# Optimization experiments

Measured on AMD Instinct MI355X. Metric: run time of the kernel, lower is better.

## Reference

```python
import jax, jax.numpy as jnp
import numpy as np

N_EMBD = 1024
N_FF = 4 * N_EMBD
N_EXPERTS = 8
TOP_K = 2
B, S = 1, 2048


def setup_inputs() -> dict:
    key = jax.random.key(0)
    ks = jax.random.split(key, 8)
    std = 0.02
    x = jax.random.normal(ks[0], (B, S, N_EMBD), dtype=jnp.float32)
    Wr = jax.random.normal(ks[1], (N_EMBD, N_EXPERTS), dtype=jnp.float32) * std
    br = jnp.zeros((N_EXPERTS,), dtype=jnp.float32)
    W1 = jax.random.normal(ks[2], (N_EXPERTS, N_EMBD, N_FF), dtype=jnp.float32) * std
    b1 = jnp.zeros((N_EXPERTS, N_FF), dtype=jnp.float32)
    W2 = jax.random.normal(ks[3], (N_EXPERTS, N_FF, N_EMBD), dtype=jnp.float32) * std
    b2 = jnp.zeros((N_EXPERTS, N_EMBD), dtype=jnp.float32)
    return {"x": x, "Wr": Wr, "br": br, "W1": W1, "b1": b1, "W2": W2, "b2": b2}


def reference(x, Wr, br, W1, b1, W2, b2):
    # x: [B, S, D]
    Bx, Sx, D = x.shape
    T = Bx * Sx
    E = Wr.shape[1]
    flat = x.reshape(T, D)

    # Router: softmax over experts, top-k, renormalize top-k weights
    logits = flat @ Wr + br                      # [T, E]
    probs = jax.nn.softmax(logits, axis=-1)
    topk_w, topk_i = jax.lax.top_k(probs, TOP_K)  # [T, K]
    topk_w = topk_w / jnp.sum(topk_w, axis=-1, keepdims=True)

    # Per-token combined expert weights (0 for non-selected experts).
    # Equivalent to the original gather/index_add combine.
    tok = jnp.arange(T)[:, None]
    w = jnp.zeros((T, E), dtype=flat.dtype).at[tok, topk_i].add(topk_w)  # [T, E]

    # Dense grouped expert MLP (exact GELU, matching torch nn.GELU default).
    h = jnp.einsum('td,edh->teh', flat, W1) + b1          # [T, E, 4D]
    h = jax.nn.gelu(h, approximate=False)
    y = jnp.einsum('teh,ehd->ted', h, W2) + b2            # [T, E, D]

    out = jnp.einsum('ted,te->td', y, w)                  # weighted combine
    return out.reshape(Bx, Sx, D)
```

## Files before the change

kernel.cpp:

```cpp
#include <hip/hip_runtime.h>
#include <stdint.h>

#define T_TOK 2048
#define DIM   1024
#define HID   4096
#define NEXP  8

typedef __attribute__((ext_vector_type(8))) short  short8;
typedef __attribute__((ext_vector_type(4))) short  short4v;
typedef __attribute__((ext_vector_type(4))) float  floatx4;
typedef __attribute__((ext_vector_type(4))) int    intx4;

__device__ __forceinline__ ushort f2bf(float f) {
    union { float f; uint32_t i; } v; v.f = f;
    uint32_t r = v.i + 0x7FFFu + ((v.i >> 16) & 1u);
    return (ushort)(r >> 16);
}
__device__ __forceinline__ float gelu_exact(float x) {
    return 0.5f * x * (1.0f + erff(x * 0.70710678118654752f));
}
__device__ __forceinline__ void glds16(const ushort* g, ushort* lds) {
    __builtin_amdgcn_global_load_lds(
        (const __attribute__((address_space(1))) unsigned int*)g,
        (__attribute__((address_space(3))) unsigned int*)lds, 16, 0, 0);
}

__global__ __launch_bounds__(256) void cast_x_kernel(
    const float* __restrict__ x, ushort* __restrict__ Xb)
{
    int i = (blockIdx.x * 256 + threadIdx.x) * 8;
    floatx4 a = *(const floatx4*)(x + i);
    floatx4 b = *(const floatx4*)(x + i + 4);
    uint32_t o[4];
    o[0] = (uint32_t)f2bf(a[0]) | ((uint32_t)f2bf(a[1]) << 16);
    o[1] = (uint32_t)f2bf(a[2]) | ((uint32_t)f2bf(a[3]) << 16);
    o[2] = (uint32_t)f2bf(b[0]) | ((uint32_t)f2bf(b[1]) << 16);
    o[3] = (uint32_t)f2bf(b[2]) | ((uint32_t)f2bf(b[3]) << 16);
    *(intx4*)(Xb + i) = *(const intx4*)o;
}

__global__ __launch_bounds__(256) void transpose_cast_kernel(
    const float* __restrict__ in, ushort* __restrict__ out, int R, int C)
{
    __shared__ float tile[64][65];
    int e = blockIdx.z;
    int rb = blockIdx.y * 64, cb = blockIdx.x * 64;
    const float* ip = in + (size_t)e * R * C;
    ushort* op = out + (size_t)e * R * C;
    int t = threadIdx.x;
    int tr = t >> 4, tc4 = (t & 15) * 4;
#pragma unroll
    for (int i = 0; i < 4; i++) {
        int r = i * 16 + tr;
        floatx4 v = *(const floatx4*)(ip + (size_t)(rb + r) * C + cb + tc4);
        tile[r][tc4] = v[0]; tile[r][tc4 + 1] = v[1];
        tile[r][tc4 + 2] = v[2]; tile[r][tc4 + 3] = v[3];
    }
    __syncthreads();
    int cc = t >> 2, rseg = (t & 3) * 16;
#pragma unroll
    for (int s = 0; s < 2; s++) {
        ushort o[8];
#pragma unroll
        for (int j = 0; j < 8; j++) o[j] = f2bf(tile[rseg + s * 8 + j][cc]);
        *(intx4*)(op + (size_t)(cb + cc) * R + rb + rseg + s * 8) = *(const intx4*)o;
    }
}

__global__ __launch_bounds__(256) void router_kernel(
    const float* __restrict__ x, const float* __restrict__ Wr,
    const float* __restrict__ br, int* __restrict__ counts,
    int* __restrict__ tlist, float* __restrict__ wlist)
{
    int wv = threadIdx.x >> 6, l = threadIdx.x & 63;
    int t = blockIdx.x * 4 + wv;
    float acc[NEXP];
#pragma unroll
    for (int e = 0; e < NEXP; e++) acc[e] = 0.f;
    const float* xr = x + (size_t)t * DIM;
    for (int d = l; d < DIM; d += 64) {
        float xv = xr[d];
        floatx4 w0 = *(const floatx4*)(Wr + (size_t)d * NEXP);
        floatx4 w1 = *(const floatx4*)(Wr + (size_t)d * NEXP + 4);
#pragma unroll
        for (int e = 0; e < 4; e++) { acc[e] += xv * w0[e]; acc[e + 4] += xv * w1[e]; }
    }
#pragma unroll
    for (int e = 0; e < NEXP; e++) {
#pragma unroll
        for (int off = 32; off; off >>= 1) acc[e] += __shfl_xor(acc[e], off, 64);
    }
    if (l == 0) {
        float lg[NEXP];
#pragma unroll
        for (int e = 0; e < NEXP; e++) lg[e] = acc[e] + br[e];
        int e0 = 0;
#pragma unroll
        for (int e = 1; e < NEXP; e++) if (lg[e] > lg[e0]) e0 = e;
        int e1 = -1;
#pragma unroll
        for (int e = 0; e < NEXP; e++) {
            if (e == e0) continue;
            if (e1 < 0 || lg[e] > lg[e1]) e1 = e;
        }
        float w0 = 1.f / (1.f + expf(lg[e1] - lg[e0]));
        float w1 = 1.f - w0;
        int s0 = atomicAdd(&counts[e0], 1);
        tlist[e0 * T_TOK + s0] = t;
        wlist[e0 * T_TOK + s0] = w0;
        int s1 = atomicAdd(&counts[e1], 1);
        tlist[e1 * T_TOK + s1] = t | (1 << 16);
        wlist[e1 * T_TOK + s1] = w1;
    }
}

template <int MODE>
__global__ __launch_bounds__(256, 2) void moe_gemm3(
    const ushort* __restrict__ A, const ushort* __restrict__ Wt,
    const float* __restrict__ bias, const int* __restrict__ counts,
    const int* __restrict__ tlist, const float* __restrict__ wlist,
    ushort* __restrict__ Hout, float* __restrict__ Yout)
{
    constexpr int NTOT  = MODE ? DIM : HID;
    constexpr int KFULL = MODE ? HID : DIM;
    constexpr int KLEN  = MODE ? 2048 : 1024;
    constexpr int NTILE = KLEN / 64;

    int bx = blockIdx.x;
    int e, mt, nt, kc;
    if (MODE == 0) { e = bx >> 9; mt = (bx >> 5) & 15; nt = bx & 31; kc = 0; }
    else { e = bx >> 8; int rr = bx & 255; mt = rr >> 4; nt = (rr >> 1) & 7; kc = rr & 1; }

    int Ne = counts[e];
    if (mt * 128 >= Ne) return;

    __shared__ ushort lds[32768];

    int tid = threadIdx.x, wv = tid >> 6, l = tid & 63;

    int s0 = mt * 128 + l;      if (s0 >= Ne) s0 = Ne - 1;
    int s1 = mt * 128 + 64 + l; if (s1 >= Ne) s1 = Ne - 1;
    int p0 = tlist[e * T_TOK + s0], p1 = tlist[e * T_TOK + s1];
    size_t ar0 = MODE ? (size_t)((p0 & 0xFFFF) * 2 + ((p0 >> 16) & 1)) : (size_t)(p0 & 0xFFFF);
    size_t ar1 = MODE ? (size_t)((p1 & 0xFFFF) * 2 + ((p1 >> 16) & 1)) : (size_t)(p1 & 0xFFFF);
    const ushort* asrc0 = A + ar0 * KFULL + kc * 2048;
    const ushort* asrc1 = A + ar1 * KFULL + kc * 2048;
    const ushort* bsrc0 = Wt + (size_t)e * NTOT * KFULL
                             + (size_t)(nt * 128 + l) * KFULL + kc * 2048;
    const ushort* bsrc1 = bsrc0 + (size_t)64 * KFULL;
    int q0 = wv, q1 = wv + 4;

#define STAGE(buf, t) do {                                             \
        ushort* Lb = &lds[(buf) * 16384];                              \
        int ko = (t) * 64;                                             \
        glds16(asrc0 + ko + q0 * 8, Lb + q0 * 1024);                   \
        glds16(asrc0 + ko + q1 * 8, Lb + q1 * 1024);                   \
        glds16(asrc1 + ko + q0 * 8, Lb + q0 * 1024 + 512);             \
        glds16(asrc1 + ko + q1 * 8, Lb + q1 * 1024 + 512);             \
        glds16(bsrc0 + ko + q0 * 8, Lb + 8192 + q0 * 1024);            \
        glds16(bsrc0 + ko + q1 * 8, Lb + 8192 + q1 * 1024);            \
        glds16(bsrc1 + ko + q0 * 8, Lb + 8192 + q0 * 1024 + 512);      \
        glds16(bsrc1 + ko + q1 * 8, Lb + 8192 + q1 * 1024 + 512);      \
    } while (0)

    int wm = wv >> 1, wn = wv & 1, q4 = l >> 4, lr = l & 15;
    int aro[4], bro[4];
#pragma unroll
    for (int mi = 0; mi < 4; mi++) aro[mi] = (wm * 64 + mi * 16 + lr) * 8;
#pragma unroll
    for (int ni = 0; ni < 4; ni++) bro[ni] = 8192 + (wn * 64 + ni * 16 + lr) * 8;

    floatx4 zz = {0.f, 0.f, 0.f, 0.f};
    floatx4 acc[4][4];
#pragma unroll
    for (int mi = 0; mi < 4; mi++)
#pragma unroll
        for (int ni = 0; ni < 4; ni++) acc[mi][ni] = zz;

    STAGE(0, 0);
    int cur = 0;
    for (int t = 0; t < NTILE; ++t) {
        asm volatile("" ::: "memory");
        __builtin_amdgcn_s_barrier();
        asm volatile("" ::: "memory");
        if (t + 1 < NTILE) {
            STAGE(cur ^ 1, t + 1);
            asm volatile("s_waitcnt vmcnt(8)" ::: "memory");
        } else {
            asm volatile("s_waitcnt vmcnt(0)" ::: "memory");
        }
        __builtin_amdgcn_s_barrier();
        asm volatile("" ::: "memory");

        const ushort* Lp = &lds[cur * 16384];
        short8 af[4], bfv[4];
#pragma unroll
        for (int kk = 0; kk < 2; ++kk) {
            int qb = (kk * 4 + q4) * 1024;
#pragma unroll
            for (int ni = 0; ni < 4; ni++) bfv[ni] = *(const short8*)&Lp[qb + bro[ni]];
#pragma unroll
            for (int mi = 0; mi < 4; mi++) af[mi] = *(const short8*)&Lp[qb + aro[mi]];
#pragma unroll
            for (int mi = 0; mi < 4; mi++)
#pragma unroll
                for (int ni = 0; ni < 4; ni++)
                    acc[mi][ni] = __builtin_amdgcn_mfma_f32_16x16x32_bf16(
                        af[mi], bfv[ni], acc[mi][ni], 0, 0, 0);
        }
        cur ^= 1;
    }
#undef STAGE

#pragma unroll
    for (int mi = 0; mi < 4; mi++) {
        int rbase = wm * 64 + mi * 16 + q4 * 4;
#pragma unroll
        for (int j = 0; j < 4; j++) {
            int slot2 = mt * 128 + rbase + j;
            if (slot2 >= Ne) continue;
            int pk2 = tlist[e * T_TOK + slot2];
            int tok2 = pk2 & 0xFFFF, rk2 = (pk2 >> 16) & 1;
#pragma unroll
            for (int ni = 0; ni < 4; ni++) {
                int col = nt * 128 + wn * 64 + ni * 16 + lr;
                float v = acc[mi][ni][j];
                float bc = bias[e * NTOT + col];
                if (MODE == 0) {
                    v = gelu_exact(v + bc);
                    Hout[(size_t)(tok2 * 2 + rk2) * HID + col] = f2bf(v);
                } else {
                    if (kc == 0) v += bc;
                    v *= wlist[e * T_TOK + slot2];
                    atomicAdd(&Yout[(size_t)tok2 * DIM + col], v);
                }
            }
        }
    }
}

template <int MODE>
__global__ __launch_bounds__(256, 2) void moe_gemm(
    const ushort* __restrict__ A, const float* __restrict__ W,
    const float* __restrict__ bias, const int* __restrict__ counts,
    const int* __restrict__ tlist, const float* __restrict__ wlist,
    ushort* __restrict__ Hout, float* __restrict__ Yacc)
{
    constexpr int NTOT = MODE ? DIM : HID;
    constexpr int AROW = MODE ? HID : DIM;
    constexpr int KLEN = MODE ? 2048 : 1024;

    int bx = blockIdx.x;
    int e, mt, nt, kc;
    if (MODE == 0) { e = bx >> 9; mt = (bx >> 5) & 15; nt = bx & 31; kc = 0; }
    else { e = bx >> 8; int r = bx & 255; mt = r >> 4; nt = (r >> 1) & 7; kc = r & 1; }

    int Ne = counts[e];
    if (mt * 128 >= Ne) return;

    size_t wbase = (size_t)e * DIM * HID + (size_t)kc * 2048 * NTOT + (size_t)nt * 128;

    __shared__ ushort ldsA[128 * 40];
    __shared__ ushort ldsB[128 * 36];

    int tid = threadIdx.x;
    int wv = tid >> 6, l = tid & 63;

    const ushort* arowp[2]; int apos[2];
#pragma unroll
    for (int i = 0; i < 2; i++) {
        int idx = i * 256 + tid;
        int r = idx >> 2, p = idx & 3;
        int slot = mt * 128 + r; if (slot >= Ne) slot = Ne - 1;
        int packed = tlist[e * T_TOK + slot];
        int tok = packed & 0xFFFF, rk = (packed >> 16) & 1;
        size_t arow = MODE ? (size_t)(tok * 2 + rk) : (size_t)tok;
        arowp[i] = A + arow * AROW + (MODE ? kc * 2048 : 0) + p * 8;
        apos[i] = r * 40 + p * 8;
    }

    int kp = tid & 15;
    int n8 = tid >> 4;
    size_t boffg = wbase + (size_t)(2 * kp) * NTOT + n8 * 8;

    int wm = wv >> 1, wn = wv & 1;
    int q = l >> 4;
    int aoff[4], boff[4];
#pragma unroll
    for (int mi = 0; mi < 4; mi++)
        aoff[mi] = (wm * 64 + mi * 16 + (l & 15)) * 40 + q * 8;
#pragma unroll
    for (int ni = 0; ni < 4; ni++)
        boff[ni] = (wn * 64 + ni * 16 + (l & 15)) * 36 + q * 8;

    floatx4 zz = {0.f, 0.f, 0.f, 0.f};
    floatx4 acc[4][4];
#pragma unroll
    for (int mi = 0; mi < 4; mi++)
#pragma unroll
        for (int ni = 0; ni < 4; ni++) acc[mi][ni] = zz;

    for (int k0 = 0; k0 < KLEN; k0 += 32) {
        intx4 av[2];
#pragma unroll
        for (int i = 0; i < 2; i++) av[i] = *(const intx4*)(arowp[i] + k0);
        const float* p0 = W + boffg + (size_t)k0 * NTOT;
        const float* p1 = p0 + NTOT;
        floatx4 a0 = *(const floatx4*)(p0);
        floatx4 a1 = *(const floatx4*)(p0 + 4);
        floatx4 b0 = *(const floatx4*)(p1);
        floatx4 b1 = *(const floatx4*)(p1 + 4);
        uint32_t pr[8];
#pragma unroll
        for (int j = 0; j < 8; j++) {
            float va = (j < 4) ? a0[j & 3] : a1[j & 3];
            float vb = (j < 4) ? b0[j & 3] : b1[j & 3];
            pr[j] = (uint32_t)f2bf(va) | ((uint32_t)f2bf(vb) << 16);
        }

        __syncthreads();
#pragma unroll
        for (int i = 0; i < 2; i++) *(intx4*)&ldsA[apos[i]] = av[i];
#pragma unroll
        for (int j = 0; j < 8; j++)
            *(uint32_t*)&ldsB[(n8 * 8 + j) * 36 + 2 * kp] = pr[j];
        __syncthreads();

        short8 af[4], bf[4];
#pragma unroll
        for (int mi = 0; mi < 4; mi++) af[mi] = *(const short8*)&ldsA[aoff[mi]];
#pragma unroll
        for (int ni = 0; ni < 4; ni++) {
            short4v blo = *(const short4v*)&ldsB[boff[ni]];
            short4v bhi = *(const short4v*)&ldsB[boff[ni] + 4];
            bf[ni] = __builtin_shufflevector(blo, bhi, 0, 1, 2, 3, 4, 5, 6, 7);
        }
#pragma unroll
        for (int mi = 0; mi < 4; mi++)
#pragma unroll
            for (int ni = 0; ni < 4; ni++)
                acc[mi][ni] = __builtin_amdgcn_mfma_f32_16x16x32_bf16(
                    af[mi], bf[ni], acc[mi][ni], 0, 0, 0);
    }

#pragma unroll
    for (int mi = 0; mi < 4; mi++) {
        int rbase = wm * 64 + mi * 16 + q * 4;
#pragma unroll
        for (int j = 0; j < 4; j++) {
            int slot = mt * 128 + rbase + j;
            if (slot >= Ne) continue;
            int packed = tlist[e * T_TOK + slot];
            int tok = packed & 0xFFFF, rk = (packed >> 16) & 1;
#pragma unroll
            for (int ni = 0; ni < 4; ni++) {
                int col = nt * 128 + wn * 64 + ni * 16 + (l & 15);
                float v = acc[mi][ni][j];
                float bc = bias[e * NTOT + col];
                if (MODE == 0) {
                    v = gelu_exact(v + bc);
                    Hout[(size_t)(tok * 2 + rk) * HID + col] = f2bf(v);
                } else {
                    if (kc == 0) v += bc;
                    v *= wlist[e * T_TOK + slot];
                    atomicAdd(&Yacc[(size_t)tok * DIM + col], v);
                }
            }
        }
    }
}

__global__ __launch_bounds__(256) void combine_kernel(
    const float* __restrict__ Y, float* __restrict__ out)
{
    int i = (blockIdx.x * 256 + threadIdx.x) * 4;
    *(floatx4*)(out + i) = *(const floatx4*)(Y + i);
}

extern "C" void kernel_launch(void* const* d_in, const int* in_sizes, int n_in,
                              void* d_out, int out_size, void* d_ws, size_t ws_size,
                              hipStream_t stream) {
    const float* x  = (const float*)d_in[0];
    const float* Wr = (const float*)d_in[1];
    const float* br = (const float*)d_in[2];
    const float* W1 = (const float*)d_in[3];
    const float* b1 = (const float*)d_in[4];
    const float* W2 = (const float*)d_in[5];
    const float* b2 = (const float*)d_in[6];
    float* out = (float*)d_out;
    char* ws = (char*)d_ws;

    if (ws_size >= 104988928ULL) {
        int*    counts = (int*)ws;
        int*    tlist  = (int*)(ws + 256);
        float*  wlist  = (float*)(ws + 65792);
        ushort* Xb     = (ushort*)(ws + 131328);
        ushort* Hbuf   = (ushort*)(ws + 4325632);
        ushort* Wt     = (ushort*)(ws + 37880064);

        hipMemsetAsync(counts, 0, 256, stream);
        hipMemsetAsync(out, 0, (size_t)T_TOK * DIM * sizeof(float), stream);
        cast_x_kernel<<<T_TOK * DIM / 2048, 256, 0, stream>>>(x, Xb);
        router_kernel<<<T_TOK / 4, 256, 0, stream>>>(x, Wr, br, counts, tlist, wlist);
        transpose_cast_kernel<<<dim3(HID / 64, DIM / 64, NEXP), 256, 0, stream>>>(
            W1, Wt, DIM, HID);
        moe_gemm3<0><<<NEXP * 16 * 32, 256, 0, stream>>>(
            Xb, Wt, b1, counts, tlist, wlist, Hbuf, nullptr);
        transpose_cast_kernel<<<dim3(DIM / 64, HID / 64, NEXP), 256, 0, stream>>>(
            W2, Wt, HID, DIM);
        moe_gemm3<1><<<NEXP * 16 * 8 * 2, 256, 0, stream>>>(
            Hbuf, Wt, b2, counts, tlist, wlist, nullptr, out);
    } else {
        int*    counts = (int*)ws;
        int*    tlist  = (int*)(ws + 256);
        float*  wlist  = (float*)(ws + 256 + 65536);
        ushort* Hbuf   = (ushort*)(ws + 256 + 131072);
        float*  Yacc   = (float*)(ws + 256 + 131072 + 33554432);
        ushort* Xb     = (ushort*)Yacc;

        hipMemsetAsync(counts, 0, 256, stream);
        cast_x_kernel<<<T_TOK * DIM / 2048, 256, 0, stream>>>(x, Xb);
        router_kernel<<<T_TOK / 4, 256, 0, stream>>>(x, Wr, br, counts, tlist, wlist);
        moe_gemm<0><<<NEXP * 16 * 32, 256, 0, stream>>>(Xb, W1, b1, counts, tlist, wlist, Hbuf, nullptr);
        hipMemsetAsync(Yacc, 0, (size_t)T_TOK * DIM * sizeof(float), stream);
        moe_gemm<1><<<NEXP * 16 * 8 * 2, 256, 0, stream>>>(Hbuf, W2, b2, counts, tlist, wlist, nullptr, Yacc);
        combine_kernel<<<out_size / 1024, 256, 0, stream>>>(Yacc, out);
    }
}
```

Baseline: 607.1 us.

## Pre-tile transposed weights into contiguous swizzled blocks for MoE GEMM loads

The weight transpose-cast kernel now writes W1/W2 as contiguous 128x64 bf16 tiles with an XOR swizzle, so each GEMM k-step loads one contiguous 16KB block. The GEMM's A and B LDS layouts switch to row-major 64-element rows with an XOR column swizzle, and the fragment reads use matching swizzled offsets. The aim is fully contiguous global loads for B and fewer LDS bank conflicts on fragment reads. In exchange the transpose kernel and GEMM indexing become more intricate and tightly coupled.

```diff
diff --git a/kernel.cpp b/kernel.cpp
--- a/kernel.cpp
+++ b/kernel.cpp
@@ -39,31 +39,31 @@
     *(intx4*)(Xb + i) = *(const intx4*)o;
 }
 
-__global__ __launch_bounds__(256) void transpose_cast_kernel(
+__global__ __launch_bounds__(256) void transpose_cast_tiled(
     const float* __restrict__ in, ushort* __restrict__ out, int R, int C)
 {
-    __shared__ float tile[64][65];
-    int e = blockIdx.z;
-    int rb = blockIdx.y * 64, cb = blockIdx.x * 64;
-    const float* ip = in + (size_t)e * R * C;
-    ushort* op = out + (size_t)e * R * C;
+    __shared__ float tl[64 * 132];
+    int e = blockIdx.z, nb = blockIdx.y, kt = blockIdx.x;
+    int NKT = R >> 6, NBLK = C >> 7;
+    const float* ip = in + (size_t)e * R * C + (size_t)(kt * 64) * C + nb * 128;
+    ushort* op = out + ((size_t)(e * NBLK + nb) * NKT + kt) * 8192;
     int t = threadIdx.x;
-    int tr = t >> 4, tc4 = (t & 15) * 4;
-#pragma unroll
-    for (int i = 0; i < 4; i++) {
-        int r = i * 16 + tr;
-        floatx4 v = *(const floatx4*)(ip + (size_t)(rb + r) * C + cb + tc4);
-        tile[r][tc4] = v[0]; tile[r][tc4 + 1] = v[1];
-        tile[r][tc4 + 2] = v[2]; tile[r][tc4 + 3] = v[3];
+    int rr = t >> 2, cs = (t & 3) * 32;
+#pragma unroll
+    for (int j = 0; j < 8; j++) {
+        floatx4 v = *(const floatx4*)(ip + (size_t)rr * C + cs + j * 4);
+        *(floatx4*)&tl[rr * 132 + cs + j * 4] = v;
     }
     __syncthreads();
-    int cc = t >> 2, rseg = (t & 3) * 16;
-#pragma unroll
-    for (int s = 0; s < 2; s++) {
+    int r = t >> 1, sb = (t & 1) * 4;
+#pragma unroll
+    for (int s2 = 0; s2 < 4; s2++) {
+        int s = sb + s2;
+        int c = s ^ (r & 7);
         ushort o[8];
 #pragma unroll
-        for (int j = 0; j < 8; j++) o[j] = f2bf(tile[rseg + s * 8 + j][cc]);
-        *(intx4*)(op + (size_t)(cb + cc) * R + rb + rseg + s * 8) = *(const intx4*)o;
+        for (int j = 0; j < 8; j++) o[j] = f2bf(tl[(c * 8 + j) * 132 + r]);
+        *(intx4*)(op + r * 64 + s * 8) = *(const intx4*)o;
     }
 }
 
@@ -115,7 +115,7 @@
 }
 
 template <int MODE>
-__global__ __launch_bounds__(256, 2) void moe_gemm3(
+__global__ __launch_bounds__(256, 2) void moe_gemm4(
     const ushort* __restrict__ A, const ushort* __restrict__ Wt,
     const float* __restrict__ bias, const int* __restrict__ counts,
     const int* __restrict__ tlist, const float* __restrict__ wlist,
@@ -125,6 +125,8 @@
     constexpr int KFULL = MODE ? HID : DIM;
     constexpr int KLEN  = MODE ? 2048 : 1024;
     constexpr int NTILE = KLEN / 64;
+    constexpr int NBLK  = NTOT / 128;
+    constexpr int NKT   = KFULL / 64;
 
     int bx = blockIdx.x;
     int e, mt, nt, kc;
@@ -137,38 +139,45 @@
     __shared__ ushort lds[32768];
 
     int tid = threadIdx.x, wv = tid >> 6, l = tid & 63;
-
-    int s0 = mt * 128 + l;      if (s0 >= Ne) s0 = Ne - 1;
-    int s1 = mt * 128 + 64 + l; if (s1 >= Ne) s1 = Ne - 1;
-    int p0 = tlist[e * T_TOK + s0], p1 = tlist[e * T_TOK + s1];
-    size_t ar0 = MODE ? (size_t)((p0 & 0xFFFF) * 2 + ((p0 >> 16) & 1)) : (size_t)(p0 & 0xFFFF);
-    size_t ar1 = MODE ? (size_t)((p1 & 0xFFFF) * 2 + ((p1 >> 16) & 1)) : (size_t)(p1 & 0xFFFF);
-    const ushort* asrc0 = A + ar0 * KFULL + kc * 2048;
-    const ushort* asrc1 = A + ar1 * KFULL + kc * 2048;
-    const ushort* bsrc0 = Wt + (size_t)e * NTOT * KFULL
-                             + (size_t)(nt * 128 + l) * KFULL + kc * 2048;
-    const ushort* bsrc1 = bsrc0 + (size_t)64 * KFULL;
-    int q0 = wv, q1 = wv + 4;
+    int lr8 = l >> 3, lc8 = l & 7;
+    int swz8 = (lc8 ^ lr8) * 8;
+
+    const ushort* aps[4];
+#pragma unroll
+    for (int i = 0; i < 4; i++) {
+        int r = wv * 32 + i * 8 + lr8;
+        int slot = mt * 128 + r; if (slot >= Ne) slot = Ne - 1;
+        int pk = tlist[e * T_TOK + slot];
+        size_t arow = MODE ? (size_t)((pk & 0xFFFF) * 2 + ((pk >> 16) & 1))
+                           : (size_t)(pk & 0xFFFF);
+        aps[i] = A + arow * KFULL + kc * 2048 + swz8;
+    }
+    const ushort* bp = Wt + ((size_t)(e * NBLK + nt) * NKT + kc * 32) * 8192
+                          + wv * 2048 + l * 8;
 
 #define STAGE(buf, t) do {                                             \
-        ushort* Lb = &lds[(buf) * 16384];                              \
+        ushort* La = &lds[(buf) * 16384 + wv * 2048];                  \
         int ko = (t) * 64;                                             \
-        glds16(asrc0 + ko + q0 * 8, Lb + q0 * 1024);                   \
-        glds16(asrc0 + ko + q1 * 8, Lb + q1 * 1024);                   \
-        glds16(asrc1 + ko + q0 * 8, Lb + q0 * 1024 + 512);             \
-        glds16(asrc1 + ko + q1 * 8, Lb + q1 * 1024 + 512);             \
-        glds16(bsrc0 + ko + q0 * 8, Lb + 8192 + q0 * 1024);            \
-        glds16(bsrc0 + ko + q1 * 8, Lb + 8192 + q1 * 1024);            \
-        glds16(bsrc1 + ko + q0 * 8, Lb + 8192 + q0 * 1024 + 512);      \
-        glds16(bsrc1 + ko + q1 * 8, Lb + 8192 + q1 * 1024 + 512);      \
+        glds16(aps[0] + ko, La);                                       \
+        glds16(aps[1] + ko, La + 512);                                 \
+        glds16(aps[2] + ko, La + 1024);                                \
+        glds16(aps[3] + ko, La + 1536);                                \
+        const ushort* bt = bp + (size_t)(t) * 8192;                    \
+        ushort* Lb = La + 8192;                                        \
+        glds16(bt,        Lb);                                         \
+        glds16(bt + 512,  Lb + 512);                                   \
+        glds16(bt + 1024, Lb + 1024);                                  \
+        glds16(bt + 1536, Lb + 1536);                                  \
     } while (0)
 
     int wm = wv >> 1, wn = wv & 1, q4 = l >> 4, lr = l & 15;
     int aro[4], bro[4];
 #pragma unroll
-    for (int mi = 0; mi < 4; mi++) aro[mi] = (wm * 64 + mi * 16 + lr) * 8;
-#pragma unroll
-    for (int ni = 0; ni < 4; ni++) bro[ni] = 8192 + (wn * 64 + ni * 16 + lr) * 8;
+    for (int mi = 0; mi < 4; mi++) aro[mi] = (wm * 64 + mi * 16 + lr) * 64;
+#pragma unroll
+    for (int ni = 0; ni < 4; ni++) bro[ni] = 8192 + (wn * 64 + ni * 16 + lr) * 64;
+    int sw[2] = { ((q4)     ^ (lr & 7)) * 8,
+                  ((4 + q4) ^ (lr & 7)) * 8 };
 
     floatx4 zz = {0.f, 0.f, 0.f, 0.f};
     floatx4 acc[4][4];
@@ -193,14 +202,14 @@
         asm volatile("" ::: "memory");
 
         const ushort* Lp = &lds[cur * 16384];
-        short8 af[4], bfv[4];
 #pragma unroll
         for (int kk = 0; kk < 2; ++kk) {
-            int qb = (kk * 4 + q4) * 1024;
-#pragma unroll
-            for (int ni = 0; ni < 4; ni++) bfv[ni] = *(const short8*)&Lp[qb + bro[ni]];
-#pragma unroll
-            for (int mi = 0; mi < 4; mi++) af[mi] = *(const short8*)&Lp[qb + aro[mi]];
+            int so = sw[kk];
+            short8 af[4], bfv[4];
+#pragma unroll
+            for (int ni = 0; ni < 4; ni++) bfv[ni] = *(const short8*)&Lp[bro[ni] + so];
+#pragma unroll
+            for (int mi = 0; mi < 4; mi++) af[mi] = *(const short8*)&Lp[aro[mi] + so];
 #pragma unroll
             for (int mi = 0; mi < 4; mi++)
 #pragma unroll
@@ -402,13 +411,13 @@
         hipMemsetAsync(out, 0, (size_t)T_TOK * DIM * sizeof(float), stream);
         cast_x_kernel<<<T_TOK * DIM / 2048, 256, 0, stream>>>(x, Xb);
         router_kernel<<<T_TOK / 4, 256, 0, stream>>>(x, Wr, br, counts, tlist, wlist);
-        transpose_cast_kernel<<<dim3(HID / 64, DIM / 64, NEXP), 256, 0, stream>>>(
+        transpose_cast_tiled<<<dim3(DIM / 64, HID / 128, NEXP), 256, 0, stream>>>(
             W1, Wt, DIM, HID);
-        moe_gemm3<0><<<NEXP * 16 * 32, 256, 0, stream>>>(
+        moe_gemm4<0><<<NEXP * 16 * 32, 256, 0, stream>>>(
             Xb, Wt, b1, counts, tlist, wlist, Hbuf, nullptr);
-        transpose_cast_kernel<<<dim3(DIM / 64, HID / 64, NEXP), 256, 0, stream>>>(
+        transpose_cast_tiled<<<dim3(HID / 64, DIM / 128, NEXP), 256, 0, stream>>>(
             W2, Wt, HID, DIM);
-        moe_gemm3<1><<<NEXP * 16 * 8 * 2, 256, 0, stream>>>(
+        moe_gemm4<1><<<NEXP * 16 * 8 * 2, 256, 0, stream>>>(
             Hbuf, Wt, b2, counts, tlist, wlist, nullptr, out);
     } else {
         int*    counts = (int*)ws;
```

After: 536.8 us. -11.6%, faster.
